# Performance work log

Hardware: AMD Instinct MI355X
Metric: run time of the kernel (lower is better)

The kernel has to match this reference:

```python
import jax, jax.numpy as jnp
import numpy as np

IGNORE_INDEX = -100


def setup_inputs() -> dict:
    key = jax.random.key(0)
    k1, k2, k3 = jax.random.split(key, 3)
    N, H, V = 4096, 1024, 32000
    x = jax.random.normal(k1, (N, H), dtype=jnp.float32)
    # lm_head weight, laid out [H, V] so logits = x @ weight (kernel's [D, V] layout)
    weight = jax.random.normal(k2, (H, V), dtype=jnp.float32) * (1.0 / np.sqrt(H))
    target = jax.random.randint(k3, (N,), 0, V)
    # exercise the ignore_index masking path
    target = target.at[:64].set(IGNORE_INDEX)
    return {"x": x, "weight": weight, "target": target}


def reference(x, weight, target):
    # Fused linear + cross entropy, reduction='sum'.
    # logits: [N, V] (the tensor the fused kernel tiles to avoid materializing)
    logits = jnp.dot(x, weight)
    lse = jax.nn.logsumexp(logits, axis=-1)                  # [N]
    valid = target != IGNORE_INDEX                            # [N]
    safe_labels = jnp.where(valid, target, 0)
    target_logits = jnp.take_along_axis(logits, safe_labels[:, None], axis=-1)[:, 0]
    vmask = valid.astype(logits.dtype)
    losses = (lse - target_logits) * vmask                    # [N], 0 where ignored
    lse_masked = lse * vmask
    # reduction == 'sum'
    return losses.sum(), lse_masked.sum()
```

## Files before the change

kernel.cpp:

```cpp
#include <hip/hip_runtime.h>
#include <hip/hip_bf16.h>

typedef float f32x4 __attribute__((ext_vector_type(4)));
typedef int i32x4v __attribute__((ext_vector_type(4)));
typedef int i32x8v __attribute__((ext_vector_type(8)));

#define IGNORE_INDEX (-100)
#define N_ROWS 4096
#define H_DIM  1024
#define V_DIM  32000

#define BM 128
#define BN 128
#define BK 128
#define CT_NUM (V_DIM / BN)
#define RT_NUM (N_ROWS / BM)
#define SCALE1 0x7f7f7f7f

#define XB8 (N_ROWS * H_DIM / (256 * 16))
__global__ __launch_bounds__(256) void k_prep(const float* __restrict__ x,
                                              const float* __restrict__ w,
                                              unsigned char* __restrict__ x8,
                                              unsigned char* __restrict__ wT8) {
  __shared__ float tile[128][65];
  const int t = threadIdx.x;
  if (blockIdx.x < XB8) {
    size_t i = ((size_t)blockIdx.x * 256 + t) * 16;
    const float4* xp = (const float4*)(x + i);
    float4 f0 = xp[0], f1 = xp[1], f2 = xp[2], f3 = xp[3];
    int4 o;
    int r;
    r = __builtin_amdgcn_cvt_pk_fp8_f32(f0.x, f0.y, 0, false);
    r = __builtin_amdgcn_cvt_pk_fp8_f32(f0.z, f0.w, r, true);
    o.x = r;
    r = __builtin_amdgcn_cvt_pk_fp8_f32(f1.x, f1.y, 0, false);
    r = __builtin_amdgcn_cvt_pk_fp8_f32(f1.z, f1.w, r, true);
    o.y = r;
    r = __builtin_amdgcn_cvt_pk_fp8_f32(f2.x, f2.y, 0, false);
    r = __builtin_amdgcn_cvt_pk_fp8_f32(f2.z, f2.w, r, true);
    o.z = r;
    r = __builtin_amdgcn_cvt_pk_fp8_f32(f3.x, f3.y, 0, false);
    r = __builtin_amdgcn_cvt_pk_fp8_f32(f3.z, f3.w, r, true);
    o.w = r;
    *(int4*)(x8 + i) = o;
    return;
  }
  const int b = blockIdx.x - XB8;
  const int v0 = (b % (V_DIM / 64)) * 64;
  const int k0 = (b / (V_DIM / 64)) * 128;
  {
    const int vq = t & 15;
    const int kr = t >> 4;
#pragma unroll
    for (int p = 0; p < 128; p += 16) {
      float4 v = *(const float4*)(w + (size_t)(k0 + kr + p) * V_DIM + v0 + vq * 4);
      tile[kr + p][vq * 4 + 0] = v.x;
      tile[kr + p][vq * 4 + 1] = v.y;
      tile[kr + p][vq * 4 + 2] = v.z;
      tile[kr + p][vq * 4 + 3] = v.w;
    }
  }
  __syncthreads();
  {
    const int vr = t >> 2;
    const int kq2 = t & 3;
#pragma unroll
    for (int h = 0; h < 2; ++h) {
      const int d4 = kq2 + h * 4;
      int4 o;
      int r;
#pragma unroll
      for (int d = 0; d < 4; ++d) {
        r = __builtin_amdgcn_cvt_pk_fp8_f32(tile[d4 * 16 + d * 4 + 0][vr],
                                            tile[d4 * 16 + d * 4 + 1][vr], 0, false);
        r = __builtin_amdgcn_cvt_pk_fp8_f32(tile[d4 * 16 + d * 4 + 2][vr],
                                            tile[d4 * 16 + d * 4 + 3][vr], r, true);
        ((int*)&o)[d] = r;
      }
      *(int4*)(wT8 + (size_t)(v0 + vr) * H_DIM + k0 + d4 * 16) = o;
    }
  }
}

__global__ __launch_bounds__(256) void k_gemm_lse(const unsigned char* __restrict__ A,
                                                  const unsigned char* __restrict__ Bt,
                                                  float* __restrict__ m_part,
                                                  float* __restrict__ s_part) {
  __shared__ __align__(16) unsigned char sA[BM * BK];
  __shared__ __align__(16) unsigned char sB[BN * BK];
  float* maxbuf = (float*)sA;
  float* sumbuf = (float*)(sA + 2048);

  const int tid = threadIdx.x;
  const int rt = blockIdx.x;
  const int ct = blockIdx.y;
  const int m0 = rt * BM;
  const int n0 = ct * BN;

  const int w = tid >> 6;
  const int l = tid & 63;
  const int wr = w >> 1, wc = w & 1;
  const int quad = l >> 4, lc = l & 15;

  f32x4 acc[4][4];
#pragma unroll
  for (int i = 0; i < 4; ++i)
#pragma unroll
    for (int j = 0; j < 4; ++j)
      acc[i][j] = (f32x4){0.f, 0.f, 0.f, 0.f};

  const int srow = tid >> 3;
  const int scol = ((tid & 7) ^ ((tid >> 3) & 7)) * 16;
  const unsigned char* ga = A + (size_t)(m0 + srow) * H_DIM + scol;
  const unsigned char* gb = Bt + (size_t)(n0 + srow) * H_DIM + scol;
  unsigned char* da = sA + tid * 16;
  unsigned char* db = sB + tid * 16;

  const int base_r = lc * 128;
  const int sw0 = ((quad * 2) ^ (lc & 7)) * 16;
  const int sw1 = ((quad * 2 + 1) ^ (lc & 7)) * 16;

  for (int kt = 0; kt < H_DIM / BK; ++kt) {
    __syncthreads();
#pragma unroll
    for (int i = 0; i < 4; ++i) {
      __builtin_amdgcn_global_load_lds(
          (const __attribute__((address_space(1))) void*)(ga + (size_t)i * 32 * H_DIM),
          (__attribute__((address_space(3))) void*)(da + i * 4096), 16, 0, 0);
      __builtin_amdgcn_global_load_lds(
          (const __attribute__((address_space(1))) void*)(gb + (size_t)i * 32 * H_DIM),
          (__attribute__((address_space(3))) void*)(db + i * 4096), 16, 0, 0);
    }
    ga += BK; gb += BK;
    __syncthreads();

    i32x8v a_frag[4], b_frag[4];
#pragma unroll
    for (int i = 0; i < 4; ++i) {
      const unsigned char* p = sA + (wr * 4 + i) * 2048 + base_r;
      i32x4v lo = *(const i32x4v*)(p + sw0);
      i32x4v hi = *(const i32x4v*)(p + sw1);
      a_frag[i] = __builtin_shufflevector(lo, hi, 0, 1, 2, 3, 4, 5, 6, 7);
    }
#pragma unroll
    for (int j = 0; j < 4; ++j) {
      const unsigned char* p = sB + (wc * 4 + j) * 2048 + base_r;
      i32x4v lo = *(const i32x4v*)(p + sw0);
      i32x4v hi = *(const i32x4v*)(p + sw1);
      b_frag[j] = __builtin_shufflevector(lo, hi, 0, 1, 2, 3, 4, 5, 6, 7);
    }
#pragma unroll
    for (int i = 0; i < 4; ++i)
#pragma unroll
      for (int j = 0; j < 4; ++j)
        acc[i][j] = __builtin_amdgcn_mfma_scale_f32_16x16x128_f8f6f4(
            a_frag[i], b_frag[j], acc[i][j], 0, 0, 0, SCALE1, 0, SCALE1);
  }

  float rmax[4][4];
#pragma unroll
  for (int i = 0; i < 4; ++i)
#pragma unroll
    for (int r = 0; r < 4; ++r) {
      float mx = fmaxf(fmaxf(acc[i][0][r], acc[i][1][r]),
                       fmaxf(acc[i][2][r], acc[i][3][r]));
#pragma unroll
      for (int off = 1; off < 16; off <<= 1)
        mx = fmaxf(mx, __shfl_xor(mx, off, 64));
      rmax[i][r] = mx;
    }
  __syncthreads();
  if (lc == 0) {
#pragma unroll
    for (int i = 0; i < 4; ++i)
#pragma unroll
      for (int r = 0; r < 4; ++r)
        maxbuf[(wr * 64 + i * 16 + quad * 4 + r) * 2 + wc] = rmax[i][r];
  }
  __syncthreads();
  float rowmax[4][4];
#pragma unroll
  for (int i = 0; i < 4; ++i)
#pragma unroll
    for (int r = 0; r < 4; ++r) {
      int row = wr * 64 + i * 16 + quad * 4 + r;
      rowmax[i][r] = fmaxf(maxbuf[row * 2], maxbuf[row * 2 + 1]);
    }
#pragma unroll
  for (int i = 0; i < 4; ++i)
#pragma unroll
    for (int r = 0; r < 4; ++r) {
      float s = __expf(acc[i][0][r] - rowmax[i][r]) + __expf(acc[i][1][r] - rowmax[i][r]) +
                __expf(acc[i][2][r] - rowmax[i][r]) + __expf(acc[i][3][r] - rowmax[i][r]);
#pragma unroll
      for (int off = 1; off < 16; off <<= 1)
        s += __shfl_xor(s, off, 64);
      if (lc == 0) sumbuf[(wr * 64 + i * 16 + quad * 4 + r) * 2 + wc] = s;
    }
  __syncthreads();
  if (wc == 0 && lc == 0) {
#pragma unroll
    for (int i = 0; i < 4; ++i)
#pragma unroll
      for (int r = 0; r < 4; ++r) {
        int row = wr * 64 + i * 16 + quad * 4 + r;
        size_t idx = (size_t)(m0 + row) * CT_NUM + ct;
        m_part[idx] = rowmax[i][r];
        s_part[idx] = sumbuf[row * 2] + sumbuf[row * 2 + 1];
      }
  }
}

__global__ __launch_bounds__(256) void k_combine(const float* __restrict__ x,
                                                 const unsigned char* __restrict__ wT8,
                                                 const int* __restrict__ target,
                                                 const float* __restrict__ m_part,
                                                 const float* __restrict__ s_part,
                                                 float* __restrict__ blk_part) {
  __shared__ float red[8];
  const int wv = threadIdx.x >> 6;
  const int row = blockIdx.x * 4 + wv;
  const int l = threadIdx.x & 63;
  float m = -INFINITY, s = 0.f;
  for (int ctb = l; ctb < CT_NUM; ctb += 64) {
    float mj = m_part[(size_t)row * CT_NUM + ctb];
    float sj = s_part[(size_t)row * CT_NUM + ctb];
    float M = fmaxf(m, mj);
    s = s * __expf(m - M) + sj * __expf(mj - M);
    m = M;
  }
#pragma unroll
  for (int off = 1; off < 64; off <<= 1) {
    float mo = __shfl_xor(m, off, 64);
    float so = __shfl_xor(s, off, 64);
    float M = fmaxf(m, mo);
    s = s * __expf(m - M) + so * __expf(mo - M);
    m = M;
  }
  float lse = m + logf(s);
  int tgt = target[row];
  bool valid = (tgt != IGNORE_INDEX);
  int st = valid ? tgt : 0;
  const float* xr = x + (size_t)row * H_DIM + l * 16;
  int4 wv4 = *(const int4*)(wT8 + (size_t)st * H_DIM + l * 16);
  float t = 0.f;
#define ACC_DW(dw, base)                                              \
  t += xr[base + 0] * __builtin_amdgcn_cvt_f32_fp8(dw, 0);            \
  t += xr[base + 1] * __builtin_amdgcn_cvt_f32_fp8(dw, 1);            \
  t += xr[base + 2] * __builtin_amdgcn_cvt_f32_fp8(dw, 2);            \
  t += xr[base + 3] * __builtin_amdgcn_cvt_f32_fp8(dw, 3);
  ACC_DW(wv4.x, 0)
  ACC_DW(wv4.y, 4)
  ACC_DW(wv4.z, 8)
  ACC_DW(wv4.w, 12)
#undef ACC_DW
#pragma unroll
  for (int off = 1; off < 64; off <<= 1)
    t += __shfl_xor(t, off, 64);
  if (l == 0) {
    red[wv * 2]     = valid ? (lse - t) : 0.f;
    red[wv * 2 + 1] = valid ? lse : 0.f;
  }
  __syncthreads();
  if (threadIdx.x == 0) {
    blk_part[blockIdx.x * 2]     = red[0] + red[2] + red[4] + red[6];
    blk_part[blockIdx.x * 2 + 1] = red[1] + red[3] + red[5] + red[7];
  }
}

__global__ __launch_bounds__(256) void k_final(const float* __restrict__ bp,
                                               float* __restrict__ out) {
  __shared__ float ra[4], rb[4];
  float a = 0.f, b = 0.f;
  for (int i = threadIdx.x; i < N_ROWS / 4; i += 256) {
    a += bp[i * 2];
    b += bp[i * 2 + 1];
  }
#pragma unroll
  for (int off = 1; off < 64; off <<= 1) {
    a += __shfl_xor(a, off, 64);
    b += __shfl_xor(b, off, 64);
  }
  if ((threadIdx.x & 63) == 0) { ra[threadIdx.x >> 6] = a; rb[threadIdx.x >> 6] = b; }
  __syncthreads();
  if (threadIdx.x == 0) {
    out[0] = ra[0] + ra[1] + ra[2] + ra[3];
    out[1] = rb[0] + rb[1] + rb[2] + rb[3];
  }
}

extern "C" void kernel_launch(void* const* d_in, const int* in_sizes, int n_in,
                              void* d_out, int out_size, void* d_ws, size_t ws_size,
                              hipStream_t stream) {
  const float* x = (const float*)d_in[0];
  const float* w = (const float*)d_in[1];
  const int* target = (const int*)d_in[2];
  float* out = (float*)d_out;

  char* ws = (char*)d_ws;
  unsigned char* x8 = (unsigned char*)ws;
  unsigned char* wT8 = (unsigned char*)(ws + 4194304);
  float* m_part = (float*)(ws + 4194304 + 32768000);
  float* s_part = (float*)(ws + 4194304 + 32768000 + 4096000);
  float* blk_part = (float*)(ws + 4194304 + 32768000 + 4096000 + 4096000);

  k_prep<<<dim3(XB8 + (V_DIM / 64) * (H_DIM / 128)), 256, 0, stream>>>(x, w, x8, wT8);
  k_gemm_lse<<<dim3(RT_NUM, CT_NUM), 256, 0, stream>>>(x8, wT8, m_part, s_part);
  k_combine<<<dim3(N_ROWS / 4), 256, 0, stream>>>(x, wT8, target, m_part, s_part, blk_part);
  k_final<<<dim3(1), 256, 0, stream>>>(blk_part, out);
}
```

Before: 451.7 us.

## Double-buffer LDS tiles to overlap global-to-LDS loads with MFMA compute

Shared memory for the A and B tiles now has two buffers. The GEMM loop issues the direct global-to-LDS loads for the next K tile before doing the MFMA work on the current tile, and it drops one of the two barriers per iteration. The goal is to hide global load latency behind the matrix math. In exchange, LDS use per block doubles, which can lower occupancy. The overlap may also be lost if the compiler inserts conservative vmcnt waits before the LDS reads.

```diff
diff --git a/kernel.cpp b/kernel.cpp
--- a/kernel.cpp
+++ b/kernel.cpp
@@ -86,10 +86,9 @@
                                                   const unsigned char* __restrict__ Bt,
                                                   float* __restrict__ m_part,
                                                   float* __restrict__ s_part) {
-  __shared__ __align__(16) unsigned char sA[BM * BK];
-  __shared__ __align__(16) unsigned char sB[BN * BK];
-  float* maxbuf = (float*)sA;
-  float* sumbuf = (float*)(sA + 2048);
+  __shared__ __align__(16) unsigned char sMem[2][2][BM * BK];
+  float* maxbuf = (float*)&sMem[0][0][0];
+  float* sumbuf = (float*)&sMem[0][0][2048];
 
   const int tid = threadIdx.x;
   const int rt = blockIdx.x;
@@ -113,38 +112,49 @@
   const int scol = ((tid & 7) ^ ((tid >> 3) & 7)) * 16;
   const unsigned char* ga = A + (size_t)(m0 + srow) * H_DIM + scol;
   const unsigned char* gb = Bt + (size_t)(n0 + srow) * H_DIM + scol;
-  unsigned char* da = sA + tid * 16;
-  unsigned char* db = sB + tid * 16;
+  const int dOff = tid * 16;
 
   const int base_r = lc * 128;
   const int sw0 = ((quad * 2) ^ (lc & 7)) * 16;
   const int sw1 = ((quad * 2 + 1) ^ (lc & 7)) * 16;
 
+#define ISSUE_TILE(buf)                                                          \
+  do {                                                                           \
+    unsigned char* da_ = &sMem[buf][0][dOff];                                    \
+    unsigned char* db_ = &sMem[buf][1][dOff];                                    \
+    _Pragma("unroll")                                                            \
+    for (int i_ = 0; i_ < 4; ++i_) {                                             \
+      __builtin_amdgcn_global_load_lds(                                          \
+          (const __attribute__((address_space(1))) void*)(ga + (size_t)i_ * 32 * H_DIM), \
+          (__attribute__((address_space(3))) void*)(da_ + i_ * 4096), 16, 0, 0); \
+      __builtin_amdgcn_global_load_lds(                                          \
+          (const __attribute__((address_space(1))) void*)(gb + (size_t)i_ * 32 * H_DIM), \
+          (__attribute__((address_space(3))) void*)(db_ + i_ * 4096), 16, 0, 0); \
+    }                                                                            \
+    ga += BK;                                                                    \
+    gb += BK;                                                                    \
+  } while (0)
+
+  ISSUE_TILE(0);
+
+#pragma unroll
   for (int kt = 0; kt < H_DIM / BK; ++kt) {
     __syncthreads();
+    if (kt < H_DIM / BK - 1) ISSUE_TILE((kt + 1) & 1);
+
+    const unsigned char* bufA = &sMem[kt & 1][0][0];
+    const unsigned char* bufB = &sMem[kt & 1][1][0];
+    i32x8v a_frag[4], b_frag[4];
 #pragma unroll
     for (int i = 0; i < 4; ++i) {
-      __builtin_amdgcn_global_load_lds(
-          (const __attribute__((address_space(1))) void*)(ga + (size_t)i * 32 * H_DIM),
-          (__attribute__((address_space(3))) void*)(da + i * 4096), 16, 0, 0);
-      __builtin_amdgcn_global_load_lds(
-          (const __attribute__((address_space(1))) void*)(gb + (size_t)i * 32 * H_DIM),
-          (__attribute__((address_space(3))) void*)(db + i * 4096), 16, 0, 0);
-    }
-    ga += BK; gb += BK;
-    __syncthreads();
-
-    i32x8v a_frag[4], b_frag[4];
-#pragma unroll
-    for (int i = 0; i < 4; ++i) {
-      const unsigned char* p = sA + (wr * 4 + i) * 2048 + base_r;
+      const unsigned char* p = bufA + (wr * 4 + i) * 2048 + base_r;
       i32x4v lo = *(const i32x4v*)(p + sw0);
       i32x4v hi = *(const i32x4v*)(p + sw1);
       a_frag[i] = __builtin_shufflevector(lo, hi, 0, 1, 2, 3, 4, 5, 6, 7);
     }
 #pragma unroll
     for (int j = 0; j < 4; ++j) {
-      const unsigned char* p = sB + (wc * 4 + j) * 2048 + base_r;
+      const unsigned char* p = bufB + (wc * 4 + j) * 2048 + base_r;
       i32x4v lo = *(const i32x4v*)(p + sw0);
       i32x4v hi = *(const i32x4v*)(p + sw1);
       b_frag[j] = __builtin_shufflevector(lo, hi, 0, 1, 2, 3, 4, 5, 6, 7);
@@ -156,6 +166,7 @@
         acc[i][j] = __builtin_amdgcn_mfma_scale_f32_16x16x128_f8f6f4(
             a_frag[i], b_frag[j], acc[i][j], 0, 0, 0, SCALE1, 0, SCALE1);
   }
+#undef ISSUE_TILE
 
   float rmax[4][4];
 #pragma unroll
```

Result: faster. 434.2 us (-3.9%).
